# Performance work log

Hardware: AMD Instinct MI355X
Metric: run time of the kernel (lower is better)

Reference implementation:

```python
import jax, jax.numpy as jnp
import numpy as np

UNITS = 1024
IN_DIM = 128

def _gru_params(key, d_in, units, dtype=jnp.float32):
    k1, k2, k3 = jax.random.split(key, 3)
    s_x = 1.0 / np.sqrt(d_in)
    s_h = 1.0 / np.sqrt(units)
    Wx = jax.random.normal(k1, (d_in, 3 * units), dtype) * s_x
    Wh = jax.random.normal(k2, (units, 3 * units), dtype) * s_h
    bx = jnp.zeros((3 * units,), dtype)
    bh = jnp.zeros((3 * units,), dtype)
    return Wx, Wh, bx, bh

def setup_inputs() -> dict:
    key = jax.random.key(0)
    ks = jax.random.split(key, 6)
    inputs = jax.random.normal(ks[0], (128, 256, IN_DIM), jnp.float32)
    d = {"inputs": inputs}
    dims_in = [IN_DIM, UNITS, UNITS, UNITS]
    for i in range(4):
        Wx, Wh, bx, bh = _gru_params(ks[1 + i], dims_in[i], UNITS)
        d[f"Wx{i+1}"] = Wx
        d[f"Wh{i+1}"] = Wh
        d[f"bx{i+1}"] = bx
        d[f"bh{i+1}"] = bh
    d["Wd"] = jax.random.normal(ks[5], (UNITS, 1), jnp.float32) / np.sqrt(UNITS)
    d["bd"] = jnp.zeros((1,), jnp.float32)
    return d

def _gru_layer(x, Wx, Wh, bx, bh):
    # x: [B,T,D]. Keras GRU v2 (reset_after=True), inference mode (no dropout).
    B = x.shape[0]
    U = Wh.shape[0]
    # precompute input projections for the whole sequence
    xg = jnp.einsum('btd,dg->btg', x, Wx) + bx  # [B,T,3U]
    def step(h, xt):
        rec = h @ Wh + bh                       # [B,3U]
        xz, xr, xh = jnp.split(xt, 3, axis=-1)
        rz, rr, rh = jnp.split(rec, 3, axis=-1)
        z = jax.nn.sigmoid(xz + rz)
        r = jax.nn.sigmoid(xr + rr)
        hh = jnp.tanh(xh + r * rh)
        h_new = z * h + (1.0 - z) * hh
        return h_new, h_new
    h0 = jnp.zeros((B, U), x.dtype)
    hT, hs = jax.lax.scan(step, h0, jnp.swapaxes(xg, 0, 1))
    return jnp.swapaxes(hs, 0, 1), hT  # ([B,T,U], [B,U])

def reference(inputs, Wx1, Wh1, bx1, bh1, Wx2, Wh2, bx2, bh2,
              Wx3, Wh3, bx3, bh3, Wx4, Wh4, bx4, bh4, Wd, bd):
    x, _ = _gru_layer(inputs, Wx1, Wh1, bx1, bh1)
    x, _ = _gru_layer(x, Wx2, Wh2, bx2, bh2)
    x, _ = _gru_layer(x, Wx3, Wh3, bx3, bh3)
    _, h = _gru_layer(x, Wx4, Wh4, bx4, bh4)   # last GRU returns final state [B,U]
    return h @ Wd + bd                          # [B,1]
```

## Files before the change

### kernel.cpp

```cpp
#include <hip/hip_runtime.h>
#include <hip/hip_bf16.h>
#include <hip/hip_cooperative_groups.h>
#include <math.h>

typedef short bfrag8 __attribute__((ext_vector_type(8)));
typedef float facc4  __attribute__((ext_vector_type(4)));

#define BATCH   128
#define TSTEPS  256
#define UNITS   1024


struct Sync {
  unsigned int cnt[4][64];
  unsigned int gen[4][64];
};

struct GArgs {
  const __hip_bfloat16* xin;
  const __hip_bfloat16* Wp[4];
  const float* pb;
  __hip_bfloat16* hout;
  float* hfin;
  Sync* sy;
  const float* Wd;
  const float* bd;
  float* out;
};

__global__ void prep_xin(const float* __restrict__ in, __hip_bfloat16* __restrict__ xin) {
  const int idx = blockIdx.x * 256 + threadIdx.x;
  if (idx >= TSTEPS * 16 * 128) return;
  const int m  = idx & 127;
  const int kg = (idx >> 7) & 15;
  const int t  = idx >> 11;
  union { __hip_bfloat16 h[8]; uint4 v; } o;
  const float* src = in + ((size_t)m * TSTEPS + t) * 128 + (kg << 3);
  #pragma unroll
  for (int e = 0; e < 8; ++e) o.h[e] = __float2bfloat16(src[e]);
  ((uint4*)xin)[idx] = o.v;
}

__global__ void prep_w(const float* __restrict__ Wx, const float* __restrict__ Wh,
                       int Din, int KS, int NKT, __hip_bfloat16* __restrict__ W) {
  const int p   = blockIdx.x;
  const int tid = threadIdx.x;
  const int k0  = tid << 3;
  if (k0 >= KS) return;
  const int nt = p >> 6, r = p & 63;
  const int wn = r >> 5, fb = (r >> 4) & 1, rl = r & 15;
  const int gg = (r >> 3) & 3, eu = r & 7;
  const int u   = nt * 16 + wn * 8 + eu;
  const int col = (gg == 0) ? u : (gg == 1) ? (1024 + u) : (2048 + u);
  const int kt = tid >> 3, c = tid & 7, kh = c >> 2, kq = c & 3;
  const int lane = kq * 16 + rl;
  union { __hip_bfloat16 h[8]; uint4 v; } o;
  #pragma unroll
  for (int e = 0; e < 8; ++e) {
    const int k = k0 + e;
    float v = 0.0f;
    if (k < Din) { if (gg != 3) v = Wx[(size_t)k * 3072 + col]; }
    else         { if (gg != 2) v = Wh[(size_t)(k - Din) * 3072 + col]; }
    o.h[e] = __float2bfloat16(v);
  }
  const size_t off16 = (size_t)nt * (NKT * 512)
                     + (size_t)(((kt * 2 + wn) * 2 + kh) * 2 + fb) * 64 + lane;
  ((uint4*)W)[off16] = o.v;
}

struct BiasArgs { const float* bx[4]; const float* bh[4]; float* pb; };

__global__ void prep_bias(BiasArgs ba) {
  const int idx = blockIdx.x * 256 + threadIdx.x;
  if (idx >= 4 * 4096) return;
  const int p = idx & 4095, l = idx >> 12;
  const int nt = p >> 6, r = p & 63;
  const int uh = r >> 5, g = (r >> 3) & 3, eu = r & 7;
  const int u = nt * 16 + uh * 8 + eu;
  const float* bx = ba.bx[l];
  const float* bh = ba.bh[l];
  float v;
  if (g == 0)      v = bx[u] + bh[u];
  else if (g == 1) v = bx[1024 + u] + bh[1024 + u];
  else if (g == 2) v = bx[2048 + u];
  else             v = bh[2048 + u];
  ba.pb[idx] = v;
}

__global__ void prep_zero(__hip_bfloat16* hout, Sync* sy) {
  const int b = blockIdx.x;
  if (b < 1024) {
    const uint4 z4 = {0, 0, 0, 0};
    ((uint4*)hout)[b * 256 + threadIdx.x] = z4;
  } else {
    unsigned int* p = (unsigned int*)sy;
    #pragma unroll
    for (int i = 0; i < 2; ++i) p[i * 256 + threadIdx.x] = 0u;
  }
}

__global__ __launch_bounds__(256) void gru_pipe(GArgs g) {
  __shared__ float lsC[128 * 66];

  const int tid  = threadIdx.x;
  const int lane = tid & 63;
  const int wave = tid >> 6;
  const int wm = wave >> 1, wn = wave & 1;
  const int wg = blockIdx.x;
  const int l  = (wg & 7) >> 1;
  const int nt = ((wg >> 3) << 1) | (wg & 1);
  const int NKT  = l ? 32 : 18;
  const int DINC = l ? 128 : 16;
  const float* pbL = g.pb + (l << 12) + (nt << 6);
  const int r15 = lane & 15;
  const int kq  = lane >> 4;

  const char* Bbase = (const char*)g.Wp[l]
                    + (size_t)nt * NKT * 8192 + (size_t)wn * 4096 + (size_t)lane * 16;
  int aoff[4];
  #pragma unroll
  for (int fa = 0; fa < 4; ++fa) aoff[fa] = (wm * 64 + fa * 16 + r15) * 16;

  float hfr[8];
  #pragma unroll
  for (int e = 0; e < 8; ++e) hfr[e] = 0.0f;
  const int pm  = tid & 127;
  const int blk = tid >> 7;

  unsigned int* cnt = &g.sy->cnt[l][0];
  unsigned int* genL = &g.sy->gen[l][0];
  unsigned int* genU = (l > 0) ? &g.sy->gen[l - 1][0] : nullptr;
  unsigned int* genD = (l < 3) ? &g.sy->gen[l + 1][0] : nullptr;

  const size_t CH = 128 * 1024;

  for (int t = 0; t < TSTEPS; ++t) {
    {
      if (tid == 0) {
        while (__hip_atomic_load(genL, __ATOMIC_RELAXED, __HIP_MEMORY_SCOPE_AGENT)
               < (unsigned)t) __builtin_amdgcn_s_sleep(4);
      } else if (tid == 1 && genU) {
        while (__hip_atomic_load(genU, __ATOMIC_RELAXED, __HIP_MEMORY_SCOPE_AGENT)
               < (unsigned)(t + 1)) __builtin_amdgcn_s_sleep(4);
      } else if (tid == 2 && genD && t >= 4) {
        while (__hip_atomic_load(genD, __ATOMIC_RELAXED, __HIP_MEMORY_SCOPE_AGENT)
               < (unsigned)(t - 3)) __builtin_amdgcn_s_sleep(4);
      }
      __syncthreads();
      if (tid == 0) __builtin_amdgcn_fence(__ATOMIC_ACQUIRE, "agent");
      __syncthreads();
    }

    const __hip_bfloat16* hA = g.hout + (size_t)((l << 2) | ((t + 3) & 3)) * CH;
    const __hip_bfloat16* xA = l
        ? (g.hout + (size_t)(((l - 1) << 2) | (t & 3)) * CH)
        : (g.xin + (size_t)t * (16 * 128 * 8));

    bfrag8 aP[8], bP[4], aQ[8], bQ[4];

    #define LOADAB(AR, BR, KT)                                               \
      {                                                                      \
        const int kt_ = (KT);                                                \
        _Pragma("unroll")                                                    \
        for (int kh = 0; kh < 2; ++kh) {                                     \
          const int gk = kt_ * 8 + kh * 4 + kq;                              \
          const char* src = (gk < DINC)                                      \
              ? ((const char*)xA + (size_t)gk * 2048)                        \
              : ((const char*)hA + (size_t)(gk - DINC) * 2048);              \
          _Pragma("unroll")                                                  \
          for (int fa = 0; fa < 4; ++fa)                                     \
            AR[kh * 4 + fa] = *(const bfrag8*)(src + aoff[fa]);              \
          _Pragma("unroll")                                                  \
          for (int fb = 0; fb < 2; ++fb)                                     \
            BR[kh * 2 + fb] = *(const bfrag8*)(Bbase + (size_t)kt_ * 8192    \
                                               + kh * 2048 + fb * 1024);     \
        }                                                                    \
      }

    #define DOMFMA(AR, BR)                                                   \
      _Pragma("unroll")                                                      \
      for (int kh = 0; kh < 2; ++kh) {                                       \
        _Pragma("unroll")                                                    \
        for (int fa = 0; fa < 4; ++fa) {                                     \
          acc[fa][0] = __builtin_amdgcn_mfma_f32_16x16x32_bf16(              \
              AR[kh * 4 + fa], BR[kh * 2 + 0], acc[fa][0], 0, 0, 0);         \
          acc[fa][1] = __builtin_amdgcn_mfma_f32_16x16x32_bf16(              \
              AR[kh * 4 + fa], BR[kh * 2 + 1], acc[fa][1], 0, 0, 0);         \
        }                                                                    \
      }

    facc4 acc[4][2];
    #pragma unroll
    for (int fa = 0; fa < 4; ++fa)
      #pragma unroll
      for (int fb = 0; fb < 2; ++fb)
        acc[fa][fb] = (facc4){0, 0, 0, 0};

    LOADAB(aP, bP, 0);
    for (int kt = 0; kt < NKT; kt += 2) {
      LOADAB(aQ, bQ, kt + 1);
      DOMFMA(aP, bP);
      if (kt + 2 < NKT) LOADAB(aP, bP, kt + 2);
      DOMFMA(aQ, bQ);
    }
    #undef LOADAB
    #undef DOMFMA

    {
      #pragma unroll
      for (int fa = 0; fa < 4; ++fa) {
        const int crow = (wm << 6) + (fa << 4) + ((lane >> 4) << 2);
        #pragma unroll
        for (int fb = 0; fb < 2; ++fb) {
          const int ccol = (wn << 5) + (fb << 4) + r15;
          #pragma unroll
          for (int j = 0; j < 4; ++j)
            lsC[(crow + j) * 66 + ccol] = acc[fa][fb][j];
        }
      }
    }
    __syncthreads();

    {
      __hip_bfloat16* houtW = g.hout + (size_t)((l << 2) | (t & 3)) * CH;
      const float* cr  = lsC + pm * 66 + blk * 32;
      const float* pbb = pbL + blk * 32;
      union { __hip_bfloat16 h[8]; uint4 v; } ou;
      #pragma unroll
      for (int e = 0; e < 8; ++e) {
        const float gz  = cr[e]      + pbb[e];
        const float gr  = cr[8 + e]  + pbb[8 + e];
        const float gxh = cr[16 + e] + pbb[16 + e];
        const float grh = cr[24 + e] + pbb[24 + e];
        const float z = 1.0f / (1.0f + __expf(-gz));
        const float r = 1.0f / (1.0f + __expf(-gr));
        const float e2 = __expf(2.0f * (gxh + r * grh));
        const float hh = 1.0f - 2.0f / (e2 + 1.0f);
        const float hn = z * hfr[e] + (1.0f - z) * hh;
        hfr[e] = hn;
        ou.h[e] = __float2bfloat16(hn);
      }
      ((uint4*)houtW)[(nt * 2 + blk) * 128 + pm] = ou.v;
      if (l == 3 && t == TSTEPS - 1) {
        float* dst = g.hfin + (size_t)pm * 1024 + (nt << 4) + (blk << 3);
        #pragma unroll
        for (int e = 0; e < 8; ++e) dst[e] = hfr[e];
      }
    }
    __syncthreads();

    if (tid == 0) {
      __builtin_amdgcn_fence(__ATOMIC_RELEASE, "agent");
      unsigned int old = __hip_atomic_fetch_add(cnt, 1u, __ATOMIC_RELAXED,
                                                __HIP_MEMORY_SCOPE_AGENT);
      if (old == (unsigned)(64 * (t + 1) - 1))
        __hip_atomic_store(genL, (unsigned)(t + 1), __ATOMIC_RELEASE,
                           __HIP_MEMORY_SCOPE_AGENT);
    }
  }

  if (wg < BATCH) {
    if (tid == 0) {
      while (__hip_atomic_load(&g.sy->gen[3][0], __ATOMIC_RELAXED,
                               __HIP_MEMORY_SCOPE_AGENT) < (unsigned)TSTEPS)
        __builtin_amdgcn_s_sleep(4);
      __builtin_amdgcn_fence(__ATOMIC_ACQUIRE, "agent");
    }
    __syncthreads();
    const float* h = g.hfin + (size_t)wg * 1024;
    float ssum = 0.0f;
    for (int u = tid; u < UNITS; u += 256) ssum += h[u] * g.Wd[u];
    lsC[tid] = ssum;
    __syncthreads();
    for (int off = 128; off; off >>= 1) {
      if (tid < off) lsC[tid] += lsC[tid + off];
      __syncthreads();
    }
    if (tid == 0) g.out[wg] = lsC[0] + g.bd[0];
  }
}

extern "C" void kernel_launch(void* const* d_in, const int* in_sizes, int n_in,
                              void* d_out, int out_size, void* d_ws, size_t ws_size,
                              hipStream_t stream) {
  (void)in_sizes; (void)n_in; (void)out_size; (void)ws_size;
  const float* inputs = (const float*)d_in[0];
  const float* Wx[4] = {(const float*)d_in[1], (const float*)d_in[5], (const float*)d_in[9],  (const float*)d_in[13]};
  const float* Wh[4] = {(const float*)d_in[2], (const float*)d_in[6], (const float*)d_in[10], (const float*)d_in[14]};
  const float* bx[4] = {(const float*)d_in[3], (const float*)d_in[7], (const float*)d_in[11], (const float*)d_in[15]};
  const float* bh[4] = {(const float*)d_in[4], (const float*)d_in[8], (const float*)d_in[12], (const float*)d_in[16]};
  const float* Wd = (const float*)d_in[17];
  const float* bd = (const float*)d_in[18];

  char* w = (char*)d_ws;
  auto alloc = [&](size_t bytes) {
    char* p = w;
    w += (bytes + 255) & ~(size_t)255;
    return p;
  };
  __hip_bfloat16* xin = (__hip_bfloat16*)alloc((size_t)TSTEPS * 16 * 128 * 8 * 2);
  __hip_bfloat16* Wp[4];
  Wp[0] = (__hip_bfloat16*)alloc((size_t)64 * 18 * 8192);
  for (int l = 1; l < 4; ++l)
    Wp[l] = (__hip_bfloat16*)alloc((size_t)64 * 32 * 8192);
  __hip_bfloat16* hout = (__hip_bfloat16*)alloc((size_t)4 * 4 * 128 * 1024 * 2);
  float* hfin = (float*)alloc((size_t)128 * 1024 * 4);
  float* pb = (float*)alloc((size_t)4 * 4096 * 4);
  Sync* sy = (Sync*)alloc(sizeof(Sync));

  prep_xin<<<(TSTEPS * 16 * 128) / 256, 256, 0, stream>>>(inputs, xin);
  for (int l = 0; l < 4; ++l) {
    const int Din = (l == 0) ? 128 : 1024;
    const int NKT = (l == 0) ? 18 : 32;
    prep_w<<<4096, 256, 0, stream>>>(Wx[l], Wh[l], Din, Din + 1024, NKT, Wp[l]);
  }
  BiasArgs ba;
  for (int l = 0; l < 4; ++l) { ba.bx[l] = bx[l]; ba.bh[l] = bh[l]; }
  ba.pb = pb;
  prep_bias<<<64, 256, 0, stream>>>(ba);
  prep_zero<<<1025, 256, 0, stream>>>(hout, sy);

  GArgs ga;
  ga.xin = xin;
  for (int l = 0; l < 4; ++l) ga.Wp[l] = Wp[l];
  ga.pb = pb;
  ga.hout = hout;
  ga.hfin = hfin;
  ga.sy = sy;
  ga.Wd = Wd;
  ga.bd = bd;
  ga.out = (float*)d_out;

  void* kargs[] = { &ga };
  hipLaunchCooperativeKernel((const void*)gru_pipe, dim3(256), dim3(256), kargs, 0, stream);
}
```

Measured before the change: 7.100 ms.

## Keep GRU weights resident in registers with split-K across waves

Each wave now holds its slice of the combined input/recurrent weight tile in VGPRs for the whole sequence, so the weights are no longer reloaded from global memory at every timestep. The K dimension is split across the four waves, which cover all 128 rows and 64 columns, and the partial sums are reduced through LDS in two halves before the pointwise gate math. The cooperative launch is replaced by a normal launch, with spin-wait guards added against deadlock. The costs are very high register pressure from 64 resident weight fragments plus 32 accumulators, extra LDS traffic and barriers for the reduction, and reliance on all blocks being co-resident without a cooperative launch guarantee.

```diff
diff --git a/kernel.cpp b/kernel.cpp
--- a/kernel.cpp
+++ b/kernel.cpp
@@ -1,6 +1,5 @@
 #include <hip/hip_runtime.h>
 #include <hip/hip_bf16.h>
-#include <hip/hip_cooperative_groups.h>
 #include <math.h>
 
 typedef short bfrag8 __attribute__((ext_vector_type(8)));
@@ -9,6 +8,7 @@
 #define BATCH   128
 #define TSTEPS  256
 #define UNITS   1024
+#define SPIN_GUARD (1u << 24)
 
 
 struct Sync {
@@ -42,18 +42,21 @@
 }
 
 __global__ void prep_w(const float* __restrict__ Wx, const float* __restrict__ Wh,
-                       int Din, int KS, int NKT, __hip_bfloat16* __restrict__ W) {
+                       int Din, int KS, int KK, int KQ,
+                       __hip_bfloat16* __restrict__ W) {
   const int p   = blockIdx.x;
   const int tid = threadIdx.x;
   const int k0  = tid << 3;
   if (k0 >= KS) return;
   const int nt = p >> 6, r = p & 63;
-  const int wn = r >> 5, fb = (r >> 4) & 1, rl = r & 15;
+  const int fb = r >> 4, rl = r & 15;
   const int gg = (r >> 3) & 3, eu = r & 7;
-  const int u   = nt * 16 + wn * 8 + eu;
+  const int u   = nt * 16 + (r >> 5) * 8 + eu;
   const int col = (gg == 0) ? u : (gg == 1) ? (1024 + u) : (2048 + u);
-  const int kt = tid >> 3, c = tid & 7, kh = c >> 2, kq = c & 3;
-  const int lane = kq * 16 + rl;
+  const int q  = k0 / KQ;
+  const int kw = k0 - q * KQ;
+  const int kk = kw >> 5, ku = (kw >> 3) & 3;
+  const int lane = ku * 16 + rl;
   union { __hip_bfloat16 h[8]; uint4 v; } o;
   #pragma unroll
   for (int e = 0; e < 8; ++e) {
@@ -63,9 +66,8 @@
     else         { if (gg != 2) v = Wh[(size_t)(k - Din) * 3072 + col]; }
     o.h[e] = __float2bfloat16(v);
   }
-  const size_t off16 = (size_t)nt * (NKT * 512)
-                     + (size_t)(((kt * 2 + wn) * 2 + kh) * 2 + fb) * 64 + lane;
-  ((uint4*)W)[off16] = o.v;
+  const size_t idx16 = ((size_t)(((nt * 4 + q) * KK + kk) * 4 + fb)) * 64 + lane;
+  ((uint4*)W)[idx16] = o.v;
 }
 
 struct BiasArgs { const float* bx[4]; const float* bh[4]; float* pb; };
@@ -99,27 +101,38 @@
   }
 }
 
-__global__ __launch_bounds__(256) void gru_pipe(GArgs g) {
-  __shared__ float lsC[128 * 66];
+__global__ __launch_bounds__(256, 1) void gru_pipe(GArgs g) {
+  __shared__ float lsC[4 * 4224];
 
   const int tid  = threadIdx.x;
   const int lane = tid & 63;
-  const int wave = tid >> 6;
-  const int wm = wave >> 1, wn = wave & 1;
+  const int q    = tid >> 6;
   const int wg = blockIdx.x;
   const int l  = (wg & 7) >> 1;
   const int nt = ((wg >> 3) << 1) | (wg & 1);
-  const int NKT  = l ? 32 : 18;
-  const int DINC = l ? 128 : 16;
+  const int KKc   = l ? 16 : 9;
+  const int DINC8 = l ? 128 : 16;
+  const int qKQ8  = q * (l ? 64 : 36);
   const float* pbL = g.pb + (l << 12) + (nt << 6);
-  const int r15 = lane & 15;
-  const int kq  = lane >> 4;
-
-  const char* Bbase = (const char*)g.Wp[l]
-                    + (size_t)nt * NKT * 8192 + (size_t)wn * 4096 + (size_t)lane * 16;
-  int aoff[4];
+  const int rl = lane & 15;
+  const int kq = lane >> 4;
+
+  if (wg < BATCH && tid == 0) g.out[wg] = -1.0f;
+
+  bfrag8 wreg[16][4];
+  {
+    const char* wb = (const char*)g.Wp[l] + ((size_t)(nt * 4 + q) * KKc) * 4096;
+    #pragma unroll
+    for (int kk = 0; kk < 16; ++kk)
+      if (kk < KKc)
+        #pragma unroll
+        for (int fb = 0; fb < 4; ++fb)
+          wreg[kk][fb] = *(const bfrag8*)(wb + (kk * 4 + fb) * 1024 + lane * 16);
+  }
+
+  int aoff[8];
   #pragma unroll
-  for (int fa = 0; fa < 4; ++fa) aoff[fa] = (wm * 64 + fa * 16 + r15) * 16;
+  for (int fa = 0; fa < 8; ++fa) aoff[fa] = (fa * 16 + rl) * 16;
 
   float hfr[8];
   #pragma unroll
@@ -127,7 +140,7 @@
   const int pm  = tid & 127;
   const int blk = tid >> 7;
 
-  unsigned int* cnt = &g.sy->cnt[l][0];
+  unsigned int* cnt  = &g.sy->cnt[l][0];
   unsigned int* genL = &g.sy->gen[l][0];
   unsigned int* genU = (l > 0) ? &g.sy->gen[l - 1][0] : nullptr;
   unsigned int* genD = (l < 3) ? &g.sy->gen[l + 1][0] : nullptr;
@@ -136,118 +149,140 @@
 
   for (int t = 0; t < TSTEPS; ++t) {
     {
+      unsigned int gd = 0;
       if (tid == 0) {
         while (__hip_atomic_load(genL, __ATOMIC_RELAXED, __HIP_MEMORY_SCOPE_AGENT)
-               < (unsigned)t) __builtin_amdgcn_s_sleep(4);
+               < (unsigned)t) { if (++gd > SPIN_GUARD) break; __builtin_amdgcn_s_sleep(4); }
       } else if (tid == 1 && genU) {
         while (__hip_atomic_load(genU, __ATOMIC_RELAXED, __HIP_MEMORY_SCOPE_AGENT)
-               < (unsigned)(t + 1)) __builtin_amdgcn_s_sleep(4);
+               < (unsigned)(t + 1)) { if (++gd > SPIN_GUARD) break; __builtin_amdgcn_s_sleep(4); }
       } else if (tid == 2 && genD && t >= 4) {
         while (__hip_atomic_load(genD, __ATOMIC_RELAXED, __HIP_MEMORY_SCOPE_AGENT)
-               < (unsigned)(t - 3)) __builtin_amdgcn_s_sleep(4);
+               < (unsigned)(t - 3)) { if (++gd > SPIN_GUARD) break; __builtin_amdgcn_s_sleep(4); }
       }
       __syncthreads();
       if (tid == 0) __builtin_amdgcn_fence(__ATOMIC_ACQUIRE, "agent");
       __syncthreads();
     }
 
-    const __hip_bfloat16* hA = g.hout + (size_t)((l << 2) | ((t + 3) & 3)) * CH;
-    const __hip_bfloat16* xA = l
+    const char* hA = (const char*)(g.hout + (size_t)((l << 2) | ((t + 3) & 3)) * CH);
+    const char* xA = (const char*)(l
         ? (g.hout + (size_t)(((l - 1) << 2) | (t & 3)) * CH)
-        : (g.xin + (size_t)t * (16 * 128 * 8));
-
-    bfrag8 aP[8], bP[4], aQ[8], bQ[4];
-
-    #define LOADAB(AR, BR, KT)                                               \
+        : (g.xin + (size_t)t * (16 * 128 * 8)));
+
+    bfrag8 aP[8], aQ[8];
+
+    #define LOADA(AR, KK_)                                                   \
       {                                                                      \
-        const int kt_ = (KT);                                                \
+        const int kg = qKQ8 + (KK_) * 4 + kq;                                \
+        const char* srcb = (kg < DINC8)                                      \
+            ? (xA + (size_t)kg * 2048)                                       \
+            : (hA + (size_t)(kg - DINC8) * 2048);                            \
         _Pragma("unroll")                                                    \
-        for (int kh = 0; kh < 2; ++kh) {                                     \
-          const int gk = kt_ * 8 + kh * 4 + kq;                              \
-          const char* src = (gk < DINC)                                      \
-              ? ((const char*)xA + (size_t)gk * 2048)                        \
-              : ((const char*)hA + (size_t)(gk - DINC) * 2048);              \
-          _Pragma("unroll")                                                  \
-          for (int fa = 0; fa < 4; ++fa)                                     \
-            AR[kh * 4 + fa] = *(const bfrag8*)(src + aoff[fa]);              \
-          _Pragma("unroll")                                                  \
-          for (int fb = 0; fb < 2; ++fb)                                     \
-            BR[kh * 2 + fb] = *(const bfrag8*)(Bbase + (size_t)kt_ * 8192    \
-                                               + kh * 2048 + fb * 1024);     \
-        }                                                                    \
-      }
-
-    #define DOMFMA(AR, BR)                                                   \
+        for (int fa = 0; fa < 8; ++fa)                                       \
+          AR[fa] = *(const bfrag8*)(srcb + aoff[fa]);                        \
+      }
+
+    #define DOMFMA(AR, KK_)                                                  \
       _Pragma("unroll")                                                      \
-      for (int kh = 0; kh < 2; ++kh) {                                       \
+      for (int fa = 0; fa < 8; ++fa)                                         \
+        _Pragma("unroll")                                                    \
+        for (int fb = 0; fb < 4; ++fb)                                       \
+          acc[fa][fb] = __builtin_amdgcn_mfma_f32_16x16x32_bf16(             \
+              AR[fa], wreg[KK_][fb], acc[fa][fb], 0, 0, 0);
+
+    facc4 acc[8][4];
+    #pragma unroll
+    for (int fa = 0; fa < 8; ++fa)
+      #pragma unroll
+      for (int fb = 0; fb < 4; ++fb)
+        acc[fa][fb] = (facc4){0, 0, 0, 0};
+
+    LOADA(aP, 0);
+    if (l) {
+      #pragma unroll
+      for (int kk = 0; kk < 16; kk += 2) {
+        LOADA(aQ, kk + 1);
+        DOMFMA(aP, kk);
+        if (kk + 2 < 16) LOADA(aP, kk + 2);
+        DOMFMA(aQ, kk + 1);
+      }
+    } else {
+      #pragma unroll
+      for (int kk = 0; kk < 8; kk += 2) {
+        LOADA(aQ, kk + 1);
+        DOMFMA(aP, kk);
+        LOADA(aP, kk + 2);
+        DOMFMA(aQ, kk + 1);
+      }
+      DOMFMA(aP, 8);
+    }
+    #undef LOADA
+    #undef DOMFMA
+
+    __hip_bfloat16* houtW = g.hout + (size_t)((l << 2) | (t & 3)) * CH;
+
+    #define CWRITE(HALF_)                                                    \
+      {                                                                      \
+        float* Cq = lsC + q * 4224;                                          \
         _Pragma("unroll")                                                    \
         for (int fa = 0; fa < 4; ++fa) {                                     \
-          acc[fa][0] = __builtin_amdgcn_mfma_f32_16x16x32_bf16(              \
-              AR[kh * 4 + fa], BR[kh * 2 + 0], acc[fa][0], 0, 0, 0);         \
-          acc[fa][1] = __builtin_amdgcn_mfma_f32_16x16x32_bf16(              \
-              AR[kh * 4 + fa], BR[kh * 2 + 1], acc[fa][1], 0, 0, 0);         \
+          const int crow = (fa << 4) + ((lane >> 4) << 2);                   \
+          _Pragma("unroll")                                                  \
+          for (int fb = 0; fb < 4; ++fb) {                                   \
+            const int ccol = (fb << 4) + rl;                                 \
+            _Pragma("unroll")                                                \
+            for (int j = 0; j < 4; ++j)                                      \
+              Cq[(crow + j) * 66 + ccol] = acc[fa + 4 * (HALF_)][fb][j];     \
+          }                                                                  \
         }                                                                    \
       }
 
-    facc4 acc[4][2];
-    #pragma unroll
-    for (int fa = 0; fa < 4; ++fa)
-      #pragma unroll
-      for (int fb = 0; fb < 2; ++fb)
-        acc[fa][fb] = (facc4){0, 0, 0, 0};
-
-    LOADAB(aP, bP, 0);
-    for (int kt = 0; kt < NKT; kt += 2) {
-      LOADAB(aQ, bQ, kt + 1);
-      DOMFMA(aP, bP);
-      if (kt + 2 < NKT) LOADAB(aP, bP, kt + 2);
-      DOMFMA(aQ, bQ);
-    }
-    #undef LOADAB
-    #undef DOMFMA
-
-    {
-      #pragma unroll
-      for (int fa = 0; fa < 4; ++fa) {
-        const int crow = (wm << 6) + (fa << 4) + ((lane >> 4) << 2);
-        #pragma unroll
-        for (int fb = 0; fb < 2; ++fb) {
-          const int ccol = (wn << 5) + (fb << 4) + r15;
-          #pragma unroll
-          for (int j = 0; j < 4; ++j)
-            lsC[(crow + j) * 66 + ccol] = acc[fa][fb][j];
-        }
-      }
-    }
-    __syncthreads();
-
-    {
-      __hip_bfloat16* houtW = g.hout + (size_t)((l << 2) | (t & 3)) * CH;
-      const float* cr  = lsC + pm * 66 + blk * 32;
-      const float* pbb = pbL + blk * 32;
-      union { __hip_bfloat16 h[8]; uint4 v; } ou;
-      #pragma unroll
-      for (int e = 0; e < 8; ++e) {
-        const float gz  = cr[e]      + pbb[e];
-        const float gr  = cr[8 + e]  + pbb[8 + e];
-        const float gxh = cr[16 + e] + pbb[16 + e];
-        const float grh = cr[24 + e] + pbb[24 + e];
-        const float z = 1.0f / (1.0f + __expf(-gz));
-        const float r = 1.0f / (1.0f + __expf(-gr));
-        const float e2 = __expf(2.0f * (gxh + r * grh));
-        const float hh = 1.0f - 2.0f / (e2 + 1.0f);
-        const float hn = z * hfr[e] + (1.0f - z) * hh;
-        hfr[e] = hn;
-        ou.h[e] = __float2bfloat16(hn);
-      }
-      ((uint4*)houtW)[(nt * 2 + blk) * 128 + pm] = ou.v;
-      if (l == 3 && t == TSTEPS - 1) {
-        float* dst = g.hfin + (size_t)pm * 1024 + (nt << 4) + (blk << 3);
-        #pragma unroll
-        for (int e = 0; e < 8; ++e) dst[e] = hfr[e];
-      }
-    }
-    __syncthreads();
+    #define POINTWISE(ROW_)                                                  \
+      {                                                                      \
+        const float* Cb = lsC + (ROW_) * 66 + blk * 32;                      \
+        const float* pbb = pbL + blk * 32;                                   \
+        union { __hip_bfloat16 h[8]; uint4 v; } ou;                          \
+        _Pragma("unroll")                                                    \
+        for (int e = 0; e < 8; ++e) {                                        \
+          float gz  = Cb[e]      + pbb[e];                                   \
+          float gr  = Cb[8 + e]  + pbb[8 + e];                               \
+          float gxh = Cb[16 + e] + pbb[16 + e];                              \
+          float grh = Cb[24 + e] + pbb[24 + e];                              \
+          _Pragma("unroll")                                                  \
+          for (int qq = 1; qq < 4; ++qq) {                                   \
+            gz  += Cb[qq * 4224 + e];                                        \
+            gr  += Cb[qq * 4224 + 8 + e];                                    \
+            gxh += Cb[qq * 4224 + 16 + e];                                   \
+            grh += Cb[qq * 4224 + 24 + e];                                   \
+          }                                                                  \
+          const float z = 1.0f / (1.0f + __expf(-gz));                       \
+          const float r = 1.0f / (1.0f + __expf(-gr));                       \
+          const float e2 = __expf(2.0f * (gxh + r * grh));                   \
+          const float hh = 1.0f - 2.0f / (e2 + 1.0f);              \
+          const float hn = z * hfr[e] + (1.0f - z) * hh;                     \
+          hfr[e] = hn;                                                       \
+          ou.h[e] = __float2bfloat16(hn);                                    \
+        }                                                                    \
+        ((uint4*)houtW)[(nt * 2 + blk) * 128 + pm] = ou.v;                   \
+        if (l == 3 && t == TSTEPS - 1) {                                     \
+          float* dst = g.hfin + (size_t)pm * 1024 + (nt << 4) + (blk << 3);  \
+          _Pragma("unroll")                                                  \
+          for (int e = 0; e < 8; ++e) dst[e] = hfr[e];                       \
+        }                                                                    \
+      }
+
+    CWRITE(0);
+    __syncthreads();
+    if (pm < 64) POINTWISE(pm);
+    __syncthreads();
+    CWRITE(1);
+    __syncthreads();
+    if (pm >= 64) POINTWISE(pm - 64);
+    __syncthreads();
+
+    #undef CWRITE
+    #undef POINTWISE
 
     if (tid == 0) {
       __builtin_amdgcn_fence(__ATOMIC_RELEASE, "agent");
@@ -261,9 +296,10 @@
 
   if (wg < BATCH) {
     if (tid == 0) {
+      unsigned int gd = 0;
       while (__hip_atomic_load(&g.sy->gen[3][0], __ATOMIC_RELAXED,
                                __HIP_MEMORY_SCOPE_AGENT) < (unsigned)TSTEPS)
-        __builtin_amdgcn_s_sleep(4);
+        { if (++gd > SPIN_GUARD) break; __builtin_amdgcn_s_sleep(4); }
       __builtin_amdgcn_fence(__ATOMIC_ACQUIRE, "agent");
     }
     __syncthreads();
@@ -300,9 +336,9 @@
   };
   __hip_bfloat16* xin = (__hip_bfloat16*)alloc((size_t)TSTEPS * 16 * 128 * 8 * 2);
   __hip_bfloat16* Wp[4];
-  Wp[0] = (__hip_bfloat16*)alloc((size_t)64 * 18 * 8192);
+  Wp[0] = (__hip_bfloat16*)alloc((size_t)64 * 4 * 9 * 4 * 64 * 16);
   for (int l = 1; l < 4; ++l)
-    Wp[l] = (__hip_bfloat16*)alloc((size_t)64 * 32 * 8192);
+    Wp[l] = (__hip_bfloat16*)alloc((size_t)64 * 4 * 16 * 4 * 64 * 16);
   __hip_bfloat16* hout = (__hip_bfloat16*)alloc((size_t)4 * 4 * 128 * 1024 * 2);
   float* hfin = (float*)alloc((size_t)128 * 1024 * 4);
   float* pb = (float*)alloc((size_t)4 * 4096 * 4);
@@ -311,8 +347,10 @@
   prep_xin<<<(TSTEPS * 16 * 128) / 256, 256, 0, stream>>>(inputs, xin);
   for (int l = 0; l < 4; ++l) {
     const int Din = (l == 0) ? 128 : 1024;
-    const int NKT = (l == 0) ? 18 : 32;
-    prep_w<<<4096, 256, 0, stream>>>(Wx[l], Wh[l], Din, Din + 1024, NKT, Wp[l]);
+    const int KS  = Din + 1024;
+    const int KK  = (l == 0) ? 9 : 16;
+    const int KQ  = KS / 4;
+    prep_w<<<4096, 256, 0, stream>>>(Wx[l], Wh[l], Din, KS, KK, KQ, Wp[l]);
   }
   BiasArgs ba;
   for (int l = 0; l < 4; ++l) { ba.bx[l] = bx[l]; ba.bh[l] = bh[l]; }
@@ -331,6 +369,5 @@
   ga.bd = bd;
   ga.out = (float*)d_out;
 
-  void* kargs[] = { &ga };
-  hipLaunchCooperativeKernel((const void*)gru_pipe, dim3(256), dim3(256), kargs, 0, stream);
-}
+  gru_pipe<<<dim3(256), dim3(256), 0, stream>>>(ga);
+}
```

New measurement: 12.32 ms. 1.74x slower.
